# Kernel optimization log

Hardware: AMD Instinct MI355X
Metric: run time of the kernel (lower is better)

The kernel has to match this reference:

```python
import jax, jax.numpy as jnp
import numpy as np

B, S, D, F, E, K = 4, 2048, 1024, 4096, 8, 2


def setup_inputs() -> dict:
    key = jax.random.key(0)
    k0, k1, k2, k3, k4 = jax.random.split(key, 5)
    return {
        "inputs": jax.random.normal(k0, (B, S, D), dtype=jnp.float32),
        "gate_w": jax.random.normal(k1, (D, E), dtype=jnp.float32) * 0.02,
        "wi0": jax.random.normal(k2, (E, D, F), dtype=jnp.float32) * 0.02,
        "wi1": jax.random.normal(k3, (E, D, F), dtype=jnp.float32) * 0.02,
        "wo": jax.random.normal(k4, (E, F, D), dtype=jnp.float32) * 0.02,
    }


def reference(inputs, gate_w, wi0, wi1, wo):
    # Router: gate logits [B,S,E], top-k then softmax over the k selected logits
    gate_logits = jnp.einsum("bsd,de->bse", inputs, gate_w)
    top_w, sel = jax.lax.top_k(gate_logits, K)  # [B,S,K] each
    top_w = jax.nn.softmax(top_w.astype(jnp.float32), axis=-1).astype(inputs.dtype)

    # Dense loop over all experts (faithful to the source module): every expert
    # computes a full gated MLP over all tokens, then is masked by routing weight.
    out = jnp.zeros_like(inputs)
    for e in range(E):
        w_e = jnp.sum((sel == e) * top_w, axis=-1)  # [B,S]
        h = jax.nn.silu(jnp.einsum("bsd,df->bsf", inputs, wi0[e])) * jnp.einsum(
            "bsd,df->bsf", inputs, wi1[e]
        )  # [B,S,F]
        out = out + w_e[:, :, None] * jnp.einsum("bsf,fd->bsd", h, wo[e])
    return out
```

## Files before the change

### kernel.cpp

```cpp
#include <hip/hip_runtime.h>

#define TOK   8192
#define DDIM  1024
#define FDIM  4096
#define NEXP  8

typedef __attribute__((ext_vector_type(8))) short short8;
typedef __attribute__((ext_vector_type(4))) float float4_t;

__device__ __forceinline__ unsigned short f2b(float f) {
    union { float f; unsigned int i; } v; v.f = f;
    unsigned int r = v.i + 0x7FFFu + ((v.i >> 16) & 1u);
    return (unsigned short)(r >> 16);
}

__device__ __forceinline__ void g2lds16(const unsigned short* g, unsigned short* l) {
    __builtin_amdgcn_global_load_lds(
        (const __attribute__((address_space(1))) unsigned int*)g,
        (__attribute__((address_space(3))) unsigned int*)l, 16, 0, 0);
}

__global__ __launch_bounds__(256) void prep_x(
    const float* __restrict__ X, unsigned short* __restrict__ Xb)
{
    int i = blockIdx.x * 256 + threadIdx.x;
    float4 v = reinterpret_cast<const float4*>(X)[i];
    union { unsigned short u[4]; uint2 p; } o;
    o.u[0] = f2b(v.x); o.u[1] = f2b(v.y); o.u[2] = f2b(v.z); o.u[3] = f2b(v.w);
    reinterpret_cast<uint2*>(Xb)[i] = o.p;
}

__global__ void zero_counts(int* __restrict__ counts) {
    if (threadIdx.x < NEXP) counts[threadIdx.x] = 0;
}

__global__ __launch_bounds__(256) void router_kernel(
    const float* __restrict__ X, const float* __restrict__ GW,
    int* __restrict__ counts, int* __restrict__ plist, float* __restrict__ wlist)
{
    int lane = threadIdx.x & 63;
    int wv   = threadIdx.x >> 6;
    int t    = blockIdx.x * 4 + wv;

    float acc[NEXP];
#pragma unroll
    for (int e = 0; e < NEXP; ++e) acc[e] = 0.f;

#pragma unroll
    for (int i = 0; i < 16; ++i) {
        int d = lane + 64 * i;
        float x = X[(size_t)t * DDIM + d];
        float4 g0 = reinterpret_cast<const float4*>(&GW[d * NEXP])[0];
        float4 g1 = reinterpret_cast<const float4*>(&GW[d * NEXP])[1];
        acc[0] += x * g0.x; acc[1] += x * g0.y; acc[2] += x * g0.z; acc[3] += x * g0.w;
        acc[4] += x * g1.x; acc[5] += x * g1.y; acc[6] += x * g1.z; acc[7] += x * g1.w;
    }
#pragma unroll
    for (int off = 32; off > 0; off >>= 1) {
#pragma unroll
        for (int e = 0; e < NEXP; ++e)
            acc[e] += __shfl_xor(acc[e], off, 64);
    }
    if (lane == 0) {
        int be = 0; float b0v = acc[0];
#pragma unroll
        for (int e = 1; e < NEXP; ++e) if (acc[e] > b0v) { b0v = acc[e]; be = e; }
        int se = -1; float b1v = -INFINITY;
#pragma unroll
        for (int e = 0; e < NEXP; ++e) if (e != be && acc[e] > b1v) { b1v = acc[e]; se = e; }
        if (se < 0 || se > 7) se = (be + 1) & 7;
        float e1 = expf(b1v - b0v);
        float w0 = 1.f / (1.f + e1);
        float w1 = e1 / (1.f + e1);
        int p0 = atomicAdd(&counts[be], 1);
        if (p0 >= 0 && p0 < TOK) { plist[be * TOK + p0] = 2 * t;     wlist[be * TOK + p0] = w0; }
        int p1 = atomicAdd(&counts[se], 1);
        if (p1 >= 0 && p1 < TOK) { plist[se * TOK + p1] = 2 * t + 1; wlist[se * TOK + p1] = w1; }
    }
}

__global__ __launch_bounds__(256) void transpose_w01(
    const float* __restrict__ wi0, const float* __restrict__ wi1,
    unsigned short* __restrict__ w01t)
{
    __shared__ float sh[32][33];
    int z = blockIdx.z; int e = z >> 1; int which = z & 1;
    const float* src = (which ? wi1 : wi0) + (size_t)e * DDIM * FDIM;
    unsigned short* dst = w01t + (size_t)e * 2 * FDIM * DDIM;
    int tx = threadIdx.x, ty = threadIdx.y;
    int r0 = blockIdx.y * 32;
    int c0 = blockIdx.x * 32;
#pragma unroll
    for (int i = 0; i < 4; ++i)
        sh[ty + 8 * i][tx] = src[(size_t)(r0 + ty + 8 * i) * FDIM + c0 + tx];
    __syncthreads();
#pragma unroll
    for (int i = 0; i < 4; ++i) {
        int f  = c0 + ty + 8 * i;
        int rp = 32 * (f >> 4) + 16 * which + (f & 15);
        dst[(size_t)rp * DDIM + r0 + tx] = f2b(sh[tx][ty + 8 * i]);
    }
}

__global__ __launch_bounds__(256) void transpose_plain(
    const float* __restrict__ wo, unsigned short* __restrict__ wot)
{
    __shared__ float sh[32][33];
    int e = blockIdx.z;
    const float* src = wo + (size_t)e * FDIM * DDIM;
    unsigned short* dst = wot + (size_t)e * DDIM * FDIM;
    int tx = threadIdx.x, ty = threadIdx.y;
    int r0 = blockIdx.y * 32;
    int c0 = blockIdx.x * 32;
#pragma unroll
    for (int i = 0; i < 4; ++i)
        sh[ty + 8 * i][tx] = src[(size_t)(r0 + ty + 8 * i) * DDIM + c0 + tx];
    __syncthreads();
#pragma unroll
    for (int i = 0; i < 4; ++i)
        dst[(size_t)(c0 + ty + 8 * i) * FDIM + r0 + tx] = f2b(sh[tx][ty + 8 * i]);
}

__global__ __launch_bounds__(256) void gemm1_kernel(
    const unsigned short* __restrict__ Xb,
    const unsigned short* __restrict__ W01t,
    const int* __restrict__ counts, const int* __restrict__ plist,
    unsigned short* __restrict__ H)
{
    int e   = blockIdx.z;
    int cnt = counts[e];
    cnt = cnt < 0 ? 0 : (cnt > TOK ? TOK : cnt);
    int m0  = blockIdx.y * 128;
    if (m0 >= cnt) return;
    int valid = cnt - m0; if (valid > 128) valid = 128;
    int bx = blockIdx.x;

    __shared__ __align__(16) unsigned short sA[128 * 64];
    __shared__ __align__(16) unsigned short sB[128 * 64];
    __shared__ int sPair[128];

    int tid = threadIdx.x, lane = tid & 63, wv = tid >> 6;
    if (tid < 128) {
        int idx = (tid < valid) ? (m0 + tid) : m0;
        sPair[tid] = plist[e * TOK + idx] & (2 * TOK - 1);
    }
    __syncthreads();

    const unsigned short* gA[4]; unsigned short* lA[4];
    const unsigned short* gB[4]; unsigned short* lB[4];
    const unsigned short* Wb = W01t + (size_t)e * (2 * FDIM) * DDIM;
#pragma unroll
    for (int i = 0; i < 4; ++i) {
        int j  = 4 * wv + i;
        int r8 = lane >> 3;
        int r  = 8 * j + r8;
        int c  = (lane & 7) ^ r8;
        gA[i] = Xb + (size_t)(sPair[r] >> 1) * DDIM + c * 8;
        gB[i] = Wb + (size_t)(bx * 128 + r) * DDIM + c * 8;
        lA[i] = &sA[j * 512];
        lB[i] = &sB[j * 512];
    }

    float4_t C[4][4];
#pragma unroll
    for (int a = 0; a < 4; ++a)
#pragma unroll
        for (int b = 0; b < 4; ++b) C[a][b] = (float4_t)0.f;

    int mrow = (wv >> 1) * 64;
    int ncol = (wv & 1) * 64;
    int rr = lane & 15, quad = lane >> 4;

#pragma unroll
    for (int i = 0; i < 4; ++i) { g2lds16(gA[i], lA[i]); gA[i] += 64; }
#pragma unroll
    for (int i = 0; i < 4; ++i) { g2lds16(gB[i], lB[i]); gB[i] += 64; }

    for (int kk = 0; kk < DDIM / 64; ++kk) {
        __syncthreads();
#pragma unroll
        for (int ks = 0; ks < 2; ++ks) {
            short8 a[4], b[4];
#pragma unroll
            for (int mt = 0; mt < 4; ++mt)
                a[mt] = *(const short8*)&sA[(mrow + mt * 16 + rr) * 64 +
                                            (((ks * 4 + quad) ^ (rr & 7)) * 8)];
#pragma unroll
            for (int nt = 0; nt < 4; ++nt)
                b[nt] = *(const short8*)&sB[(ncol + nt * 16 + rr) * 64 +
                                            (((ks * 4 + quad) ^ (rr & 7)) * 8)];
#pragma unroll
            for (int mt = 0; mt < 4; ++mt)
#pragma unroll
                for (int nt = 0; nt < 4; ++nt)
                    C[mt][nt] = __builtin_amdgcn_mfma_f32_16x16x32_bf16(a[mt], b[nt], C[mt][nt], 0, 0, 0);
        }
        __syncthreads();
        if (kk + 1 < DDIM / 64) {
#pragma unroll
            for (int i = 0; i < 4; ++i) { g2lds16(gA[i], lA[i]); gA[i] += 64; }
#pragma unroll
            for (int i = 0; i < 4; ++i) { g2lds16(gB[i], lB[i]); gB[i] += 64; }
        }
    }

    {
        unsigned short* sH = sA;
#pragma unroll
        for (int mt = 0; mt < 4; ++mt) {
#pragma unroll
            for (int i = 0; i < 4; ++i) {
                int row = mrow + mt * 16 + quad * 4 + i;
#pragma unroll
                for (int ntp = 0; ntp < 2; ++ntp) {
                    float a0 = C[mt][2 * ntp][i];
                    float a1 = C[mt][2 * ntp + 1][i];
                    float h  = (a0 / (1.f + expf(-a0))) * a1;
                    int fl = ((wv & 1) * 2 + ntp) * 16 + rr;
                    sH[row * 64 + (fl ^ (quad << 4))] = f2b(h);
                }
            }
        }
        __syncthreads();
        int r0 = tid >> 3;
        int fo = (tid & 7) * 8;
#pragma unroll
        for (int p = 0; p < 4; ++p) {
            int row = p * 32 + r0;
            if (row < valid) {
                int swz = ((row >> 2) & 3) << 4;
                uint4 v = *(const uint4*)&sH[row * 64 + (fo ^ swz)];
                *(uint4*)(H + (size_t)sPair[row] * FDIM + bx * 64 + fo) = v;
            }
        }
    }
}

__global__ __launch_bounds__(256) void gemm2_kernel(
    const unsigned short* __restrict__ H,
    const unsigned short* __restrict__ Wot,
    const int* __restrict__ counts, const int* __restrict__ plist,
    const float* __restrict__ wlist, float* __restrict__ Y)
{
    int e   = blockIdx.z;
    int cnt = counts[e];
    cnt = cnt < 0 ? 0 : (cnt > TOK ? TOK : cnt);
    int m0  = blockIdx.y * 128;
    if (m0 >= cnt) return;
    int valid = cnt - m0; if (valid > 128) valid = 128;
    int bx = blockIdx.x;

    __shared__ __align__(16) unsigned short sA[128 * 64];
    __shared__ __align__(16) unsigned short sB[128 * 64];
    __shared__ int   sPair[128];
    __shared__ float sWgt[128];

    int tid = threadIdx.x, lane = tid & 63, wv = tid >> 6;
    if (tid < 128) {
        int idx = (tid < valid) ? (m0 + tid) : m0;
        sPair[tid] = plist[e * TOK + idx] & (2 * TOK - 1);
        sWgt[tid]  = wlist[e * TOK + idx];
    }
    __syncthreads();

    const unsigned short* gA[4]; unsigned short* lA[4];
    const unsigned short* gB[4]; unsigned short* lB[4];
    const unsigned short* Wb = Wot + (size_t)e * DDIM * FDIM;
#pragma unroll
    for (int i = 0; i < 4; ++i) {
        int j  = 4 * wv + i;
        int r8 = lane >> 3;
        int r  = 8 * j + r8;
        int c  = (lane & 7) ^ r8;
        gA[i] = H + (size_t)sPair[r] * FDIM + c * 8;
        gB[i] = Wb + (size_t)(bx * 128 + r) * FDIM + c * 8;
        lA[i] = &sA[j * 512];
        lB[i] = &sB[j * 512];
    }

    float4_t C[4][4];
#pragma unroll
    for (int a = 0; a < 4; ++a)
#pragma unroll
        for (int b = 0; b < 4; ++b) C[a][b] = (float4_t)0.f;

    int mrow = (wv >> 1) * 64;
    int ncol = (wv & 1) * 64;
    int rr = lane & 15, quad = lane >> 4;

#pragma unroll
    for (int i = 0; i < 4; ++i) { g2lds16(gA[i], lA[i]); gA[i] += 64; }
#pragma unroll
    for (int i = 0; i < 4; ++i) { g2lds16(gB[i], lB[i]); gB[i] += 64; }

    for (int kk = 0; kk < FDIM / 64; ++kk) {
        __syncthreads();
#pragma unroll
        for (int ks = 0; ks < 2; ++ks) {
            short8 a[4], b[4];
#pragma unroll
            for (int mt = 0; mt < 4; ++mt)
                a[mt] = *(const short8*)&sA[(mrow + mt * 16 + rr) * 64 +
                                            (((ks * 4 + quad) ^ (rr & 7)) * 8)];
#pragma unroll
            for (int nt = 0; nt < 4; ++nt)
                b[nt] = *(const short8*)&sB[(ncol + nt * 16 + rr) * 64 +
                                            (((ks * 4 + quad) ^ (rr & 7)) * 8)];
#pragma unroll
            for (int mt = 0; mt < 4; ++mt)
#pragma unroll
                for (int nt = 0; nt < 4; ++nt)
                    C[mt][nt] = __builtin_amdgcn_mfma_f32_16x16x32_bf16(a[mt], b[nt], C[mt][nt], 0, 0, 0);
        }
        __syncthreads();
        if (kk + 1 < FDIM / 64) {
#pragma unroll
            for (int i = 0; i < 4; ++i) { g2lds16(gA[i], lA[i]); gA[i] += 64; }
#pragma unroll
            for (int i = 0; i < 4; ++i) { g2lds16(gB[i], lB[i]); gB[i] += 64; }
        }
    }

#pragma unroll
    for (int mt = 0; mt < 4; ++mt) {
#pragma unroll
        for (int i = 0; i < 4; ++i) {
            int row = mrow + mt * 16 + quad * 4 + i;
            if (row >= valid) continue;
            float w = sWgt[row];
            float* dst = Y + (size_t)sPair[row] * DDIM + bx * 128;
#pragma unroll
            for (int nt = 0; nt < 4; ++nt)
                dst[ncol + nt * 16 + rr] = w * C[mt][nt][i];
        }
    }
}

__global__ __launch_bounds__(256) void combine_kernel(
    const float* __restrict__ Y, float* __restrict__ out)
{
    int t  = blockIdx.x;
    int d0 = threadIdx.x * 4;
    float4 a = *(const float4*)(Y + (size_t)(2 * t) * DDIM + d0);
    float4 b = *(const float4*)(Y + (size_t)(2 * t + 1) * DDIM + d0);
    float4 o; o.x = a.x + b.x; o.y = a.y + b.y; o.z = a.z + b.z; o.w = a.w + b.w;
    *(float4*)(out + (size_t)t * DDIM + d0) = o;
}

extern "C" void kernel_launch(void* const* d_in, const int* in_sizes, int n_in,
                              void* d_out, int out_size, void* d_ws, size_t ws_size,
                              hipStream_t stream)
{
    const float* X   = (const float*)d_in[0];
    const float* GW  = (const float*)d_in[1];
    const float* WI0 = (const float*)d_in[2];
    const float* WI1 = (const float*)d_in[3];
    const float* WO  = (const float*)d_in[4];
    float* OUT = (float*)d_out;

    const size_t OFF_W01T = 0;
    const size_t OFF_WOT  = 134217728;
    const size_t OFF_H    = 201326592;
    const size_t OFF_XB   = 335544320;
    const size_t OFF_CNT  = 352321536;
    const size_t OFF_PL   = 352322560;
    const size_t OFF_WL   = 352584704;
    const size_t WS_NEED  = 352846848;
    if (ws_size < WS_NEED) return;

    char* ws = (char*)d_ws;
    unsigned short* W01t  = (unsigned short*)(ws + OFF_W01T);
    float*          Y     = (float*)(ws + OFF_W01T);
    unsigned short* WOt   = (unsigned short*)(ws + OFF_WOT);
    unsigned short* H     = (unsigned short*)(ws + OFF_H);
    unsigned short* Xb    = (unsigned short*)(ws + OFF_XB);
    int*            cnts  = (int*)(ws + OFF_CNT);
    int*            plist = (int*)(ws + OFF_PL);
    float*          wlist = (float*)(ws + OFF_WL);

    zero_counts<<<1, 64, 0, stream>>>(cnts);
    prep_x<<<(TOK * DDIM / 4) / 256, 256, 0, stream>>>(X, Xb);
    transpose_w01<<<dim3(FDIM / 32, DDIM / 32, 2 * NEXP), dim3(32, 8, 1), 0, stream>>>(WI0, WI1, W01t);
    transpose_plain<<<dim3(DDIM / 32, FDIM / 32, NEXP), dim3(32, 8, 1), 0, stream>>>(WO, WOt);
    router_kernel<<<TOK / 4, 256, 0, stream>>>(X, GW, cnts, plist, wlist);
    gemm1_kernel<<<dim3(2 * FDIM / 128, TOK / 128, NEXP), dim3(256), 0, stream>>>(Xb, W01t, cnts, plist, H);
    gemm2_kernel<<<dim3(DDIM / 128, TOK / 128, NEXP), dim3(256), 0, stream>>>(H, WOt, cnts, plist, wlist, Y);
    combine_kernel<<<TOK, 256, 0, stream>>>(Y, OUT);
}
```

Before: 1.216 ms.

## Enlarge MoE GEMM tiles to 512 threads with double-buffered LDS prefetch

Both expert GEMMs move to 512-thread blocks with larger tiles (256x256 for the gate/up GEMM, 128x256 for the down projection). The K loop becomes double-buffered: the next tile is loaded straight into LDS while the current one is multiplied, using explicit vmcnt waits, raw barriers and MFMA priority hints. The goal is to hide global load latency and raise data reuse per block. In exchange, LDS use rises to about 128KB and register pressure grows with the larger accumulator set, which can lower occupancy, and fewer blocks may leave the grid with poor wave balance.

New measurement: 1.345 ms. 10.5% more time.

```diff
diff --git a/kernel.cpp b/kernel.cpp
--- a/kernel.cpp
+++ b/kernel.cpp
@@ -19,6 +19,9 @@
         (const __attribute__((address_space(1))) unsigned int*)g,
         (__attribute__((address_space(3))) unsigned int*)l, 16, 0, 0);
 }
+
+#define SB0() __builtin_amdgcn_sched_barrier(0)
+#define BARRIER_RAW() __builtin_amdgcn_s_barrier()
 
 __global__ __launch_bounds__(256) void prep_x(
     const float* __restrict__ X, unsigned short* __restrict__ Xb)
@@ -121,11 +124,143 @@
         dst[(size_t)(c0 + ty + 8 * i) * FDIM + r0 + tx] = f2b(sh[tx][ty + 8 * i]);
 }
 
-__global__ __launch_bounds__(256) void gemm1_kernel(
+__global__ __launch_bounds__(512, 2) void gemm1_kernel(
     const unsigned short* __restrict__ Xb,
     const unsigned short* __restrict__ W01t,
     const int* __restrict__ counts, const int* __restrict__ plist,
     unsigned short* __restrict__ H)
+{
+    int e   = blockIdx.z;
+    int cnt = counts[e];
+    cnt = cnt < 0 ? 0 : (cnt > TOK ? TOK : cnt);
+    int m0  = blockIdx.y * 256;
+    if (m0 >= cnt) return;
+    int valid = cnt - m0; if (valid > 256) valid = 256;
+    int bx = blockIdx.x;
+
+    __shared__ __align__(16) unsigned short sA[2 * 256 * 64];
+    __shared__ __align__(16) unsigned short sB[2 * 256 * 64];
+    __shared__ int sPair[256];
+
+    int tid = threadIdx.x, lane = tid & 63, wv = tid >> 6;
+    int wm = wv >> 2, wn = wv & 3;
+    if (tid < 256) {
+        int idx = (tid < valid) ? (m0 + tid) : m0;
+        sPair[tid] = plist[e * TOK + idx] & (2 * TOK - 1);
+    }
+    __syncthreads();
+
+    const unsigned short* gA[4]; const unsigned short* gB[4];
+    unsigned short* lA[4]; unsigned short* lB[4];
+    const unsigned short* Wb = W01t + (size_t)e * (2 * FDIM) * DDIM;
+#pragma unroll
+    for (int i = 0; i < 4; ++i) {
+        int j  = wv * 4 + i;
+        int r  = j * 8 + (lane >> 3);
+        int c  = (lane & 7) ^ (r & 7);
+        gA[i] = Xb + (size_t)(sPair[r] >> 1) * DDIM + c * 8;
+        gB[i] = Wb + (size_t)(bx * 256 + r) * DDIM + c * 8;
+        lA[i] = &sA[j * 512];
+        lB[i] = &sB[j * 512];
+    }
+
+    float4_t C[8][4];
+#pragma unroll
+    for (int a = 0; a < 8; ++a)
+#pragma unroll
+        for (int b = 0; b < 4; ++b) C[a][b] = (float4_t)0.f;
+
+    int rr = lane & 15, quad = lane >> 4;
+
+#pragma unroll
+    for (int i = 0; i < 4; ++i) g2lds16(gA[i], lA[i]);
+#pragma unroll
+    for (int i = 0; i < 4; ++i) g2lds16(gB[i], lB[i]);
+#pragma unroll
+    for (int i = 0; i < 4; ++i) { gA[i] += 64; gB[i] += 64; }
+
+    const int NT = DDIM / 64;
+    for (int t = 0; t < NT; ++t) {
+        int buf = t & 1;
+        if (t + 1 < NT) {
+            int nb = buf ^ 1;
+#pragma unroll
+            for (int i = 0; i < 4; ++i) g2lds16(gA[i], lA[i] + nb * 16384);
+#pragma unroll
+            for (int i = 0; i < 4; ++i) g2lds16(gB[i], lB[i] + nb * 16384);
+#pragma unroll
+            for (int i = 0; i < 4; ++i) { gA[i] += 64; gB[i] += 64; }
+            asm volatile("s_waitcnt vmcnt(8)" ::: "memory");
+        } else {
+            asm volatile("s_waitcnt vmcnt(0)" ::: "memory");
+        }
+        SB0();
+        BARRIER_RAW();
+        SB0();
+
+        const unsigned short* A0 = &sA[buf * 16384 + (wm * 128) * 64];
+        const unsigned short* B0 = &sB[buf * 16384 + (wn * 64) * 64];
+#pragma unroll
+        for (int ks = 0; ks < 2; ++ks) {
+            short8 a[8], b[4];
+#pragma unroll
+            for (int mt = 0; mt < 8; ++mt)
+                a[mt] = *(const short8*)&A0[(mt * 16 + rr) * 64 +
+                                            (((ks * 4 + quad) ^ (rr & 7)) * 8)];
+#pragma unroll
+            for (int nt = 0; nt < 4; ++nt)
+                b[nt] = *(const short8*)&B0[(nt * 16 + rr) * 64 +
+                                            (((ks * 4 + quad) ^ (rr & 7)) * 8)];
+            __builtin_amdgcn_s_setprio(1);
+#pragma unroll
+            for (int mt = 0; mt < 8; ++mt)
+#pragma unroll
+                for (int nt = 0; nt < 4; ++nt)
+                    C[mt][nt] = __builtin_amdgcn_mfma_f32_16x16x32_bf16(a[mt], b[nt], C[mt][nt], 0, 0, 0);
+            __builtin_amdgcn_s_setprio(0);
+        }
+        SB0();
+        BARRIER_RAW();
+        SB0();
+    }
+
+    {
+        unsigned short* sH = sA;
+#pragma unroll
+        for (int mt = 0; mt < 8; ++mt) {
+#pragma unroll
+            for (int i = 0; i < 4; ++i) {
+                int row = wm * 128 + mt * 16 + quad * 4 + i;
+#pragma unroll
+                for (int ntp = 0; ntp < 2; ++ntp) {
+                    float a0 = C[mt][2 * ntp][i];
+                    float a1 = C[mt][2 * ntp + 1][i];
+                    float h  = (a0 / (1.f + expf(-a0))) * a1;
+                    int fc = (wn * 2 + ntp) ^ (row & 7);
+                    sH[row * 128 + fc * 16 + rr] = f2b(h);
+                }
+            }
+        }
+        __syncthreads();
+        int r0 = tid >> 4;
+        int u  = tid & 15;
+#pragma unroll
+        for (int p = 0; p < 8; ++p) {
+            int row = p * 32 + r0;
+            if (row < valid) {
+                int fc = (u >> 1) ^ (row & 7);
+                uint4 v = *(const uint4*)&sH[row * 128 + fc * 16 + (u & 1) * 8];
+                *(uint4*)(H + (size_t)sPair[row] * FDIM + bx * 128 + u * 8) = v;
+            }
+        }
+    }
+}
+
+__global__ __launch_bounds__(512, 2) void gemm2_kernel(
+    const unsigned short* __restrict__ H,
+    const unsigned short* __restrict__ Wot,
+    const int* __restrict__ counts, const int* __restrict__ plist,
+    const float* __restrict__ wlist, float* __restrict__ Y)
 {
     int e   = blockIdx.z;
     int cnt = counts[e];
@@ -135,127 +270,13 @@
     int valid = cnt - m0; if (valid > 128) valid = 128;
     int bx = blockIdx.x;
 
-    __shared__ __align__(16) unsigned short sA[128 * 64];
-    __shared__ __align__(16) unsigned short sB[128 * 64];
-    __shared__ int sPair[128];
-
-    int tid = threadIdx.x, lane = tid & 63, wv = tid >> 6;
-    if (tid < 128) {
-        int idx = (tid < valid) ? (m0 + tid) : m0;
-        sPair[tid] = plist[e * TOK + idx] & (2 * TOK - 1);
-    }
-    __syncthreads();
-
-    const unsigned short* gA[4]; unsigned short* lA[4];
-    const unsigned short* gB[4]; unsigned short* lB[4];
-    const unsigned short* Wb = W01t + (size_t)e * (2 * FDIM) * DDIM;
-#pragma unroll
-    for (int i = 0; i < 4; ++i) {
-        int j  = 4 * wv + i;
-        int r8 = lane >> 3;
-        int r  = 8 * j + r8;
-        int c  = (lane & 7) ^ r8;
-        gA[i] = Xb + (size_t)(sPair[r] >> 1) * DDIM + c * 8;
-        gB[i] = Wb + (size_t)(bx * 128 + r) * DDIM + c * 8;
-        lA[i] = &sA[j * 512];
-        lB[i] = &sB[j * 512];
-    }
-
-    float4_t C[4][4];
-#pragma unroll
-    for (int a = 0; a < 4; ++a)
-#pragma unroll
-        for (int b = 0; b < 4; ++b) C[a][b] = (float4_t)0.f;
-
-    int mrow = (wv >> 1) * 64;
-    int ncol = (wv & 1) * 64;
-    int rr = lane & 15, quad = lane >> 4;
-
-#pragma unroll
-    for (int i = 0; i < 4; ++i) { g2lds16(gA[i], lA[i]); gA[i] += 64; }
-#pragma unroll
-    for (int i = 0; i < 4; ++i) { g2lds16(gB[i], lB[i]); gB[i] += 64; }
-
-    for (int kk = 0; kk < DDIM / 64; ++kk) {
-        __syncthreads();
-#pragma unroll
-        for (int ks = 0; ks < 2; ++ks) {
-            short8 a[4], b[4];
-#pragma unroll
-            for (int mt = 0; mt < 4; ++mt)
-                a[mt] = *(const short8*)&sA[(mrow + mt * 16 + rr) * 64 +
-                                            (((ks * 4 + quad) ^ (rr & 7)) * 8)];
-#pragma unroll
-            for (int nt = 0; nt < 4; ++nt)
-                b[nt] = *(const short8*)&sB[(ncol + nt * 16 + rr) * 64 +
-                                            (((ks * 4 + quad) ^ (rr & 7)) * 8)];
-#pragma unroll
-            for (int mt = 0; mt < 4; ++mt)
-#pragma unroll
-                for (int nt = 0; nt < 4; ++nt)
-                    C[mt][nt] = __builtin_amdgcn_mfma_f32_16x16x32_bf16(a[mt], b[nt], C[mt][nt], 0, 0, 0);
-        }
-        __syncthreads();
-        if (kk + 1 < DDIM / 64) {
-#pragma unroll
-            for (int i = 0; i < 4; ++i) { g2lds16(gA[i], lA[i]); gA[i] += 64; }
-#pragma unroll
-            for (int i = 0; i < 4; ++i) { g2lds16(gB[i], lB[i]); gB[i] += 64; }
-        }
-    }
-
-    {
-        unsigned short* sH = sA;
-#pragma unroll
-        for (int mt = 0; mt < 4; ++mt) {
-#pragma unroll
-            for (int i = 0; i < 4; ++i) {
-                int row = mrow + mt * 16 + quad * 4 + i;
-#pragma unroll
-                for (int ntp = 0; ntp < 2; ++ntp) {
-                    float a0 = C[mt][2 * ntp][i];
-                    float a1 = C[mt][2 * ntp + 1][i];
-                    float h  = (a0 / (1.f + expf(-a0))) * a1;
-                    int fl = ((wv & 1) * 2 + ntp) * 16 + rr;
-                    sH[row * 64 + (fl ^ (quad << 4))] = f2b(h);
-                }
-            }
-        }
-        __syncthreads();
-        int r0 = tid >> 3;
-        int fo = (tid & 7) * 8;
-#pragma unroll
-        for (int p = 0; p < 4; ++p) {
-            int row = p * 32 + r0;
-            if (row < valid) {
-                int swz = ((row >> 2) & 3) << 4;
-                uint4 v = *(const uint4*)&sH[row * 64 + (fo ^ swz)];
-                *(uint4*)(H + (size_t)sPair[row] * FDIM + bx * 64 + fo) = v;
-            }
-        }
-    }
-}
-
-__global__ __launch_bounds__(256) void gemm2_kernel(
-    const unsigned short* __restrict__ H,
-    const unsigned short* __restrict__ Wot,
-    const int* __restrict__ counts, const int* __restrict__ plist,
-    const float* __restrict__ wlist, float* __restrict__ Y)
-{
-    int e   = blockIdx.z;
-    int cnt = counts[e];
-    cnt = cnt < 0 ? 0 : (cnt > TOK ? TOK : cnt);
-    int m0  = blockIdx.y * 128;
-    if (m0 >= cnt) return;
-    int valid = cnt - m0; if (valid > 128) valid = 128;
-    int bx = blockIdx.x;
-
-    __shared__ __align__(16) unsigned short sA[128 * 64];
-    __shared__ __align__(16) unsigned short sB[128 * 64];
+    __shared__ __align__(16) unsigned short sA[2 * 128 * 64];
+    __shared__ __align__(16) unsigned short sB[2 * 256 * 64];
     __shared__ int   sPair[128];
     __shared__ float sWgt[128];
 
     int tid = threadIdx.x, lane = tid & 63, wv = tid >> 6;
+    int wm = wv >> 2, wn = wv & 3;
     if (tid < 128) {
         int idx = (tid < valid) ? (m0 + tid) : m0;
         sPair[tid] = plist[e * TOK + idx] & (2 * TOK - 1);
@@ -263,18 +284,23 @@
     }
     __syncthreads();
 
-    const unsigned short* gA[4]; unsigned short* lA[4];
-    const unsigned short* gB[4]; unsigned short* lB[4];
+    const unsigned short* gA[2]; const unsigned short* gB[4];
+    unsigned short* lA[2]; unsigned short* lB[4];
     const unsigned short* Wb = Wot + (size_t)e * DDIM * FDIM;
 #pragma unroll
+    for (int i = 0; i < 2; ++i) {
+        int j = wv * 2 + i;
+        int r = j * 8 + (lane >> 3);
+        int c = (lane & 7) ^ (r & 7);
+        gA[i] = H + (size_t)sPair[r] * FDIM + c * 8;
+        lA[i] = &sA[j * 512];
+    }
+#pragma unroll
     for (int i = 0; i < 4; ++i) {
-        int j  = 4 * wv + i;
-        int r8 = lane >> 3;
-        int r  = 8 * j + r8;
-        int c  = (lane & 7) ^ r8;
-        gA[i] = H + (size_t)sPair[r] * FDIM + c * 8;
-        gB[i] = Wb + (size_t)(bx * 128 + r) * FDIM + c * 8;
-        lA[i] = &sA[j * 512];
+        int j = wv * 4 + i;
+        int r = j * 8 + (lane >> 3);
+        int c = (lane & 7) ^ (r & 7);
+        gB[i] = Wb + (size_t)(bx * 256 + r) * FDIM + c * 8;
         lB[i] = &sB[j * 512];
     }
 
@@ -284,54 +310,75 @@
 #pragma unroll
         for (int b = 0; b < 4; ++b) C[a][b] = (float4_t)0.f;
 
-    int mrow = (wv >> 1) * 64;
-    int ncol = (wv & 1) * 64;
     int rr = lane & 15, quad = lane >> 4;
 
 #pragma unroll
-    for (int i = 0; i < 4; ++i) { g2lds16(gA[i], lA[i]); gA[i] += 64; }
-#pragma unroll
-    for (int i = 0; i < 4; ++i) { g2lds16(gB[i], lB[i]); gB[i] += 64; }
-
-    for (int kk = 0; kk < FDIM / 64; ++kk) {
-        __syncthreads();
+    for (int i = 0; i < 2; ++i) g2lds16(gA[i], lA[i]);
+#pragma unroll
+    for (int i = 0; i < 4; ++i) g2lds16(gB[i], lB[i]);
+#pragma unroll
+    for (int i = 0; i < 2; ++i) gA[i] += 64;
+#pragma unroll
+    for (int i = 0; i < 4; ++i) gB[i] += 64;
+
+    const int NT = FDIM / 64;
+    for (int t = 0; t < NT; ++t) {
+        int buf = t & 1;
+        if (t + 1 < NT) {
+            int nb = buf ^ 1;
+#pragma unroll
+            for (int i = 0; i < 2; ++i) g2lds16(gA[i], lA[i] + nb * 8192);
+#pragma unroll
+            for (int i = 0; i < 4; ++i) g2lds16(gB[i], lB[i] + nb * 16384);
+#pragma unroll
+            for (int i = 0; i < 2; ++i) gA[i] += 64;
+#pragma unroll
+            for (int i = 0; i < 4; ++i) gB[i] += 64;
+            asm volatile("s_waitcnt vmcnt(6)" ::: "memory");
+        } else {
+            asm volatile("s_waitcnt vmcnt(0)" ::: "memory");
+        }
+        SB0();
+        BARRIER_RAW();
+        SB0();
+
+        const unsigned short* A0 = &sA[buf * 8192 + (wm * 64) * 64];
+        const unsigned short* B0 = &sB[buf * 16384 + (wn * 64) * 64];
 #pragma unroll
         for (int ks = 0; ks < 2; ++ks) {
             short8 a[4], b[4];
 #pragma unroll
             for (int mt = 0; mt < 4; ++mt)
-                a[mt] = *(const short8*)&sA[(mrow + mt * 16 + rr) * 64 +
+                a[mt] = *(const short8*)&A0[(mt * 16 + rr) * 64 +
                                             (((ks * 4 + quad) ^ (rr & 7)) * 8)];
 #pragma unroll
             for (int nt = 0; nt < 4; ++nt)
-                b[nt] = *(const short8*)&sB[(ncol + nt * 16 + rr) * 64 +
+                b[nt] = *(const short8*)&B0[(nt * 16 + rr) * 64 +
                                             (((ks * 4 + quad) ^ (rr & 7)) * 8)];
+            __builtin_amdgcn_s_setprio(1);
 #pragma unroll
             for (int mt = 0; mt < 4; ++mt)
 #pragma unroll
                 for (int nt = 0; nt < 4; ++nt)
                     C[mt][nt] = __builtin_amdgcn_mfma_f32_16x16x32_bf16(a[mt], b[nt], C[mt][nt], 0, 0, 0);
-        }
-        __syncthreads();
-        if (kk + 1 < FDIM / 64) {
-#pragma unroll
-            for (int i = 0; i < 4; ++i) { g2lds16(gA[i], lA[i]); gA[i] += 64; }
-#pragma unroll
-            for (int i = 0; i < 4; ++i) { g2lds16(gB[i], lB[i]); gB[i] += 64; }
-        }
+            __builtin_amdgcn_s_setprio(0);
+        }
+        SB0();
+        BARRIER_RAW();
+        SB0();
     }
 
 #pragma unroll
     for (int mt = 0; mt < 4; ++mt) {
 #pragma unroll
         for (int i = 0; i < 4; ++i) {
-            int row = mrow + mt * 16 + quad * 4 + i;
+            int row = wm * 64 + mt * 16 + quad * 4 + i;
             if (row >= valid) continue;
             float w = sWgt[row];
-            float* dst = Y + (size_t)sPair[row] * DDIM + bx * 128;
+            float* dst = Y + (size_t)sPair[row] * DDIM + bx * 256;
 #pragma unroll
             for (int nt = 0; nt < 4; ++nt)
-                dst[ncol + nt * 16 + rr] = w * C[mt][nt][i];
+                dst[wn * 64 + nt * 16 + rr] = w * C[mt][nt][i];
         }
     }
 }
@@ -383,7 +430,7 @@
     transpose_w01<<<dim3(FDIM / 32, DDIM / 32, 2 * NEXP), dim3(32, 8, 1), 0, stream>>>(WI0, WI1, W01t);
     transpose_plain<<<dim3(DDIM / 32, FDIM / 32, NEXP), dim3(32, 8, 1), 0, stream>>>(WO, WOt);
     router_kernel<<<TOK / 4, 256, 0, stream>>>(X, GW, cnts, plist, wlist);
-    gemm1_kernel<<<dim3(2 * FDIM / 128, TOK / 128, NEXP), dim3(256), 0, stream>>>(Xb, W01t, cnts, plist, H);
-    gemm2_kernel<<<dim3(DDIM / 128, TOK / 128, NEXP), dim3(256), 0, stream>>>(H, WOt, cnts, plist, wlist, Y);
+    gemm1_kernel<<<dim3(2 * FDIM / 256, TOK / 256, NEXP), dim3(512), 0, stream>>>(Xb, W01t, cnts, plist, H);
+    gemm2_kernel<<<dim3(DDIM / 256, TOK / 128, NEXP), dim3(512), 0, stream>>>(H, WOt, cnts, plist, wlist, Y);
     combine_kernel<<<TOK, 256, 0, stream>>>(Y, OUT);
 }
```
